# Optimization experiments

Measured on AMD Instinct MI355X. Metric: run time of the kernel, lower is better.

## Reference

```python
import jax, jax.numpy as jnp
import numpy as np


def setup_inputs() -> dict:
    key = jax.random.key(0)
    k1, k2 = jax.random.split(key)
    B = 64
    K = 4096
    latent_shape = (8, 250, 16)
    latent = jax.random.normal(k1, (B,) + latent_shape, dtype=jnp.float32)
    codebook = jax.random.normal(k2, (K,) + latent_shape, dtype=jnp.float32)
    usage_count = jnp.zeros((K,), dtype=jnp.float32)
    return {"latent": latent, "codebook": codebook, "usage_count": usage_count}


def reference(latent, codebook, usage_count):
    B = latent.shape[0]
    K = codebook.shape[0]
    latent_flat = latent.reshape(B, -1).astype(jnp.float32)      # [B, D]
    codebook_flat = codebook.reshape(K, -1).astype(jnp.float32)  # [K, D]

    x2 = jnp.sum(latent_flat * latent_flat, axis=1, keepdims=True)      # [B, 1]
    c2 = jnp.sum(codebook_flat * codebook_flat, axis=1)[None, :]        # [1, K]
    xc = jnp.einsum('bd,kd->bk', latent_flat, codebook_flat)            # [B, K]
    distances = jnp.sqrt(jnp.maximum(x2 + c2 - 2.0 * xc, 0.0))          # [B, K]

    indices = jnp.argmin(distances, axis=1)                             # [B] int
    min_distances = jnp.take_along_axis(distances, indices[:, None], axis=1)[:, 0]

    quantized = codebook[indices].astype(latent.dtype)                  # [B, *latent_shape]

    # scatter-add usage count update (handles duplicate indices)
    new_usage_count = usage_count.at[indices].add(1.0)

    return quantized, indices, min_distances, new_usage_count
```

## Files before the change

### kernel.cpp

```cpp
#include <hip/hip_runtime.h>
#include <math.h>

#define D      32000
#define BNUM   64
#define KNUM   4096
#define TN     64
#define BK     64
#define LDK    72

typedef __attribute__((ext_vector_type(8)))  short  short8;
typedef __attribute__((ext_vector_type(16))) float  floatx16;

__device__ __forceinline__ unsigned short f32_bf16_rne(float f) {
    unsigned u = __float_as_uint(f);
    u += 0x7fff + ((u >> 16) & 1);
    return (unsigned short)(u >> 16);
}
__device__ __forceinline__ float bf16_f32(unsigned short h) {
    return __uint_as_float(((unsigned)h) << 16);
}
__device__ __forceinline__ void cvt_hl(const float4 v, ushort4* h, ushort4* l) {
    h->x = f32_bf16_rne(v.x); l->x = f32_bf16_rne(v.x - bf16_f32(h->x));
    h->y = f32_bf16_rne(v.y); l->y = f32_bf16_rne(v.y - bf16_f32(h->y));
    h->z = f32_bf16_rne(v.z); l->z = f32_bf16_rne(v.z - bf16_f32(h->z));
    h->w = f32_bf16_rne(v.w); l->w = f32_bf16_rne(v.w - bf16_f32(h->w));
}

__device__ __forceinline__ void barrier_arrive() {
    __builtin_amdgcn_s_barrier();
}
__device__ __forceinline__ void barrier_lds() {
    __builtin_amdgcn_s_waitcnt(0xc07f);
    __builtin_amdgcn_s_barrier();
}

__global__ __launch_bounds__(256, 4) void dist_mfma(
    const float* __restrict__ latent, const float* __restrict__ codebook,
    float* __restrict__ ws_xc, float* __restrict__ ws_c2, int dper)
{
    __shared__ __align__(16) unsigned short xs_hi[BNUM * LDK];
    __shared__ __align__(16) unsigned short xs_lo[BNUM * LDK];
    __shared__ __align__(16) unsigned short cs_hi[TN * LDK];
    __shared__ __align__(16) unsigned short cs_lo[TN * LDK];

    const int tid  = threadIdx.x;
    const int k0   = blockIdx.x * TN;
    const int d0b  = blockIdx.y * dper;
    const int nst  = dper / BK;

    const int col4  = tid & 15;
    const int rbase = tid >> 4;
    const float* aptr = latent   + (size_t)rbase * D + d0b + col4 * 4;
    const float* bptr = codebook + (size_t)(k0 + rbase) * D + d0b + col4 * 4;

    const int wave = tid >> 6, lane = tid & 63;
    const int lr = lane & 31, lh = lane >> 5;
    const int mh = (wave & 1) * 32;
    const int nh = (wave >> 1) * 32;
    const int aoff = (mh + lr) * LDK + lh * 8;
    const int boff = (nh + lr) * LDK + lh * 8;

    floatx16 acc;
#pragma unroll
    for (int i = 0; i < 16; i++) acc[i] = 0.f;
    float c2p[4] = {0.f, 0.f, 0.f, 0.f};

    float4 pa[4], pbA[4], pbB[4];

#define LOADA(DST, S)                                                          \
    if ((S) < nst) {                                                           \
        const size_t _o = (size_t)(S) * BK;                                    \
        _Pragma("unroll")                                                      \
        for (int p = 0; p < 4; p++)                                            \
            DST[p] = *(const float4*)(aptr + (size_t)(16 * p) * D + _o);       \
    }
#define LOADB(DST, S)                                                          \
    if ((S) < nst) {                                                           \
        const size_t _o = (size_t)(S) * BK;                                    \
        _Pragma("unroll")                                                      \
        for (int p = 0; p < 4; p++)                                            \
            DST[p] = *(const float4*)(bptr + (size_t)(16 * p) * D + _o);       \
    }

#define STAGE(PBC, S)                                                          \
    {                                                                          \
        _Pragma("unroll")                                                      \
        for (int p = 0; p < 4; p++)                                            \
            c2p[p] += PBC[p].x * PBC[p].x + PBC[p].y * PBC[p].y +              \
                      PBC[p].z * PBC[p].z + PBC[p].w * PBC[p].w;               \
        barrier_arrive();                     \
        _Pragma("unroll")                                                      \
        for (int p = 0; p < 4; p++) {                                          \
            const int wo = (rbase + 16 * p) * LDK + col4 * 4;                  \
            ushort4 h, l;                                                      \
            cvt_hl(pa[p], &h, &l);                                             \
            *(ushort4*)(xs_hi + wo) = h;                                       \
            *(ushort4*)(xs_lo + wo) = l;                                       \
            cvt_hl(PBC[p], &h, &l);                                            \
            *(ushort4*)(cs_hi + wo) = h;                                       \
            *(ushort4*)(cs_lo + wo) = l;                                       \
        }                                                                      \
        LOADA(pa, (S) + 1);       \
        LOADB(PBC, (S) + 2);        \
        barrier_lds();                                                         \
        _Pragma("unroll")                                                      \
        for (int ks = 0; ks < 4; ++ks) {                                       \
            const short8 ah = *(const short8*)(xs_hi + aoff + ks * 16);        \
            const short8 al = *(const short8*)(xs_lo + aoff + ks * 16);        \
            const short8 bh = *(const short8*)(cs_hi + boff + ks * 16);        \
            const short8 bl = *(const short8*)(cs_lo + boff + ks * 16);        \
            acc = __builtin_amdgcn_mfma_f32_32x32x16_bf16(ah, bh, acc, 0,0,0); \
            acc = __builtin_amdgcn_mfma_f32_32x32x16_bf16(ah, bl, acc, 0,0,0); \
            acc = __builtin_amdgcn_mfma_f32_32x32x16_bf16(al, bh, acc, 0,0,0); \
        }                                                                      \
    }

    LOADA(pa, 0);
    LOADB(pbA, 0);
    LOADB(pbB, 1);

    int s = 0;
    for (; s + 1 < nst; s += 2) {
        STAGE(pbA, s);
        STAGE(pbB, s + 1);
    }
    if (s < nst) STAGE(pbA, s);

#undef STAGE
#undef LOADA
#undef LOADB

    const int split = blockIdx.y;
#pragma unroll
    for (int r = 0; r < 16; ++r) {
        const int row = (r & 3) + 8 * (r >> 2) + 4 * lh;
        const int b = mh + row;
        ws_xc[((size_t)split * BNUM + b) * KNUM + (k0 + nh + lr)] = acc[r];
    }

#pragma unroll
    for (int p = 0; p < 4; ++p) {
        float v = c2p[p];
        v += __shfl_xor(v, 1);
        v += __shfl_xor(v, 2);
        v += __shfl_xor(v, 4);
        v += __shfl_xor(v, 8);
        if ((lane & 15) == 0)
            atomicAdd(ws_c2 + k0 + rbase + 16 * p, v);
    }
}

__global__ __launch_bounds__(256) void argmin_part(
    const float* __restrict__ ws_xc, const float* __restrict__ ws_c2,
    float* __restrict__ ws_bscore, int* __restrict__ ws_bidx, int dsplit)
{
    const int b = blockIdx.x, kc = blockIdx.y, tid = threadIdx.x;
    __shared__ float sv[256];
    __shared__ int   si[256];

    float best = 3.402823466e38f;
    int   bi   = 0;
    for (int k = kc * 1024 + tid; k < (kc + 1) * 1024; k += 256) {
        float xc = 0.f;
        for (int s = 0; s < dsplit; s++)
            xc += ws_xc[((size_t)s * BNUM + b) * KNUM + k];
        const float sc = ws_c2[k] - 2.f * xc;
        if (sc < best) { best = sc; bi = k; }
    }
    sv[tid] = best; si[tid] = bi;
    __syncthreads();
    for (int off = 128; off > 0; off >>= 1) {
        if (tid < off) {
            const float ov = sv[tid + off];
            const int   oi = si[tid + off];
            if (ov < sv[tid] || (ov == sv[tid] && oi < si[tid])) {
                sv[tid] = ov; si[tid] = oi;
            }
        }
        __syncthreads();
    }
    if (tid == 0) { ws_bscore[b * 4 + kc] = sv[0]; ws_bidx[b * 4 + kc] = si[0]; }
}

__global__ __launch_bounds__(256) void finalize_k(
    const float* __restrict__ latent, const float* __restrict__ ws_bscore,
    const int* __restrict__ ws_bidx, const float* __restrict__ usage_in,
    float* __restrict__ out_idx, float* __restrict__ out_mind,
    float* __restrict__ out_usage, int* __restrict__ ws_idx)
{
    const int b = blockIdx.x, tid = threadIdx.x;
    __shared__ float sv[256];

    float s = 0.f;
    const float4* lf4 = (const float4*)(latent + (size_t)b * D);
    for (int i = tid; i < D / 4; i += 256) {
        const float4 v = lf4[i];
        s += v.x * v.x + v.y * v.y + v.z * v.z + v.w * v.w;
    }
    sv[tid] = s;
    __syncthreads();
    for (int off = 128; off > 0; off >>= 1) {
        if (tid < off) sv[tid] += sv[tid + off];
        __syncthreads();
    }
    if (tid == 0) {
        const float x2 = sv[0];
        float best = ws_bscore[b * 4];
        int   bi   = ws_bidx[b * 4];
        for (int kc = 1; kc < 4; kc++) {
            const float v = ws_bscore[b * 4 + kc];
            if (v < best) { best = v; bi = ws_bidx[b * 4 + kc]; }
        }
        out_mind[b] = sqrtf(fmaxf(x2 + best, 0.f));
        out_idx[b]  = (float)bi;
        ws_idx[b]   = bi;
    }
    if (tid < 64) out_usage[b * 64 + tid] = usage_in[b * 64 + tid];
}

__global__ __launch_bounds__(256) void gather_k(
    const float* __restrict__ codebook, const int* __restrict__ ws_idx,
    float* __restrict__ out_q, float* __restrict__ out_usage)
{
    const int b = blockIdx.x, part = blockIdx.y, tid = threadIdx.x;
    const int k = ws_idx[b];
    const int n4 = D / 4 / 4;
    const float4* src = (const float4*)(codebook + (size_t)k * D) + part * n4;
    float4*       dst = (float4*)(out_q + (size_t)b * D) + part * n4;
    for (int i = tid; i < n4; i += 256) dst[i] = src[i];
    if (part == 0 && tid == 0) atomicAdd(out_usage + k, 1.0f);
}

extern "C" void kernel_launch(void* const* d_in, const int* in_sizes, int n_in,
                              void* d_out, int out_size, void* d_ws, size_t ws_size,
                              hipStream_t stream)
{
    const float* latent   = (const float*)d_in[0];
    const float* codebook = (const float*)d_in[1];
    const float* usage    = (const float*)d_in[2];

    float* out_q     = (float*)d_out;
    float* out_idx   = out_q + (size_t)BNUM * D;
    float* out_mind  = out_idx + BNUM;
    float* out_usage = out_mind + BNUM;

    int dsplit = 20;
    if (ws_size < ((size_t)dsplit * BNUM * KNUM + KNUM + 4 * BNUM * 2 + BNUM) * 4 + 256)
        dsplit = 4;
    const int dper = D / dsplit;

    float* ws_xc     = (float*)d_ws;
    float* ws_c2     = ws_xc + (size_t)dsplit * BNUM * KNUM;
    float* ws_bscore = ws_c2 + KNUM;
    int*   ws_bidx   = (int*)(ws_bscore + 4 * BNUM);
    int*   ws_idx    = ws_bidx + 4 * BNUM;

    hipMemsetAsync(ws_c2, 0, KNUM * sizeof(float), stream);
    dist_mfma<<<dim3(KNUM / TN, dsplit), 256, 0, stream>>>(latent, codebook, ws_xc, ws_c2, dper);
    argmin_part<<<dim3(BNUM, 4), 256, 0, stream>>>(ws_xc, ws_c2, ws_bscore, ws_bidx, dsplit);
    finalize_k<<<BNUM, 256, 0, stream>>>(latent, ws_bscore, ws_bidx, usage,
                                         out_idx, out_mind, out_usage, ws_idx);
    gather_k<<<dim3(BNUM, 4), 256, 0, stream>>>(codebook, ws_idx, out_q, out_usage);
}
```

Baseline: 756.8 us.

## Preconvert latent to MFMA-ready bf16 hi/lo layout and double-buffer codebook LDS

```diff
diff --git a/kernel.cpp b/kernel.cpp
--- a/kernel.cpp
+++ b/kernel.cpp
@@ -6,7 +6,10 @@
 #define KNUM   4096
 #define TN     64
 #define BK     64
-#define LDK    72
+#define NSCB   (D / BK)
+#define AS_SCB 8192
+#define AFMT_USHORTS ((size_t)NSCB * AS_SCB)
+#define AFMT_BYTES   (AFMT_USHORTS * 2)
 
 typedef __attribute__((ext_vector_type(8)))  short  short8;
 typedef __attribute__((ext_vector_type(16))) float  floatx16;
@@ -26,109 +29,113 @@
     h->w = f32_bf16_rne(v.w); l->w = f32_bf16_rne(v.w - bf16_f32(h->w));
 }
 
-__device__ __forceinline__ void barrier_arrive() {
-    __builtin_amdgcn_s_barrier();
-}
 __device__ __forceinline__ void barrier_lds() {
     __builtin_amdgcn_s_waitcnt(0xc07f);
     __builtin_amdgcn_s_barrier();
 }
 
+__global__ __launch_bounds__(256) void conv_latent(
+    const float* __restrict__ latent, unsigned short* __restrict__ afmt)
+{
+    const int t    = blockIdx.x * 256 + threadIdx.x;
+    const int row  = t & 63;
+    const int rest = t >> 6;
+    if (rest >= NSCB * 8) return;
+    const int lh  = rest & 1;
+    const int ks  = (rest >> 1) & 3;
+    const int scb = rest >> 3;
+    const float* src = latent + (size_t)row * D + scb * 64 + ks * 16 + lh * 8;
+    const float4 v0 = *(const float4*)(src);
+    const float4 v1 = *(const float4*)(src + 4);
+    ushort4 h0, l0, h1, l1;
+    cvt_hl(v0, &h0, &l0);
+    cvt_hl(v1, &h1, &l1);
+    unsigned short* d0 = afmt + ((size_t)(rest * 2 + 0) * 64 + row) * 8;
+    unsigned short* d1 = afmt + ((size_t)(rest * 2 + 1) * 64 + row) * 8;
+    *(ushort4*)(d0)     = h0;  *(ushort4*)(d0 + 4) = h1;
+    *(ushort4*)(d1)     = l0;  *(ushort4*)(d1 + 4) = l1;
+}
+
+template<int NSTG>
 __global__ __launch_bounds__(256, 4) void dist_mfma(
-    const float* __restrict__ latent, const float* __restrict__ codebook,
-    float* __restrict__ ws_xc, float* __restrict__ ws_c2, int dper)
-{
-    __shared__ __align__(16) unsigned short xs_hi[BNUM * LDK];
-    __shared__ __align__(16) unsigned short xs_lo[BNUM * LDK];
-    __shared__ __align__(16) unsigned short cs_hi[TN * LDK];
-    __shared__ __align__(16) unsigned short cs_lo[TN * LDK];
+    const float* __restrict__ codebook, const unsigned short* __restrict__ afmt,
+    float* __restrict__ ws_xc, float* __restrict__ ws_c2)
+{
+    __shared__ __align__(16) unsigned short lds[2][2][8 * 520];
 
     const int tid  = threadIdx.x;
     const int k0   = blockIdx.x * TN;
-    const int d0b  = blockIdx.y * dper;
-    const int nst  = dper / BK;
-
-    const int col4  = tid & 15;
-    const int rbase = tid >> 4;
-    const float* aptr = latent   + (size_t)rbase * D + d0b + col4 * 4;
-    const float* bptr = codebook + (size_t)(k0 + rbase) * D + d0b + col4 * 4;
+    const int scb0 = blockIdx.y * NSTG;
+
+    const int col4 = tid & 15, rbase = tid >> 4;
+    const int cc2  = col4 >> 1, half = col4 & 1;
+    const float* bptr = codebook + (size_t)(k0 + rbase) * D
+                                 + (size_t)scb0 * 64 + col4 * 4;
 
     const int wave = tid >> 6, lane = tid & 63;
     const int lr = lane & 31, lh = lane >> 5;
-    const int mh = (wave & 1) * 32;
-    const int nh = (wave >> 1) * 32;
-    const int aoff = (mh + lr) * LDK + lh * 8;
-    const int boff = (nh + lr) * LDK + lh * 8;
+    const int mh = (wave & 1) * 32, nh = (wave >> 1) * 32;
+
+    const unsigned short* abase = afmt + (size_t)scb0 * AS_SCB
+                                       + lh * 1024 + (mh + lr) * 8;
+    const int rb_off = lh * 520 + (nh + lr) * 8;
 
     floatx16 acc;
 #pragma unroll
     for (int i = 0; i < 16; i++) acc[i] = 0.f;
     float c2p[4] = {0.f, 0.f, 0.f, 0.f};
-
-    float4 pa[4], pbA[4], pbB[4];
-
-#define LOADA(DST, S)                                                          \
-    if ((S) < nst) {                                                           \
-        const size_t _o = (size_t)(S) * BK;                                    \
-        _Pragma("unroll")                                                      \
-        for (int p = 0; p < 4; p++)                                            \
-            DST[p] = *(const float4*)(aptr + (size_t)(16 * p) * D + _o);       \
-    }
-#define LOADB(DST, S)                                                          \
-    if ((S) < nst) {                                                           \
-        const size_t _o = (size_t)(S) * BK;                                    \
-        _Pragma("unroll")                                                      \
-        for (int p = 0; p < 4; p++)                                            \
-            DST[p] = *(const float4*)(bptr + (size_t)(16 * p) * D + _o);       \
-    }
-
-#define STAGE(PBC, S)                                                          \
+    float4 pb[4];
+
+#define LOADB(S)                                                               \
     {                                                                          \
         _Pragma("unroll")                                                      \
         for (int p = 0; p < 4; p++)                                            \
-            c2p[p] += PBC[p].x * PBC[p].x + PBC[p].y * PBC[p].y +              \
-                      PBC[p].z * PBC[p].z + PBC[p].w * PBC[p].w;               \
-        barrier_arrive();                     \
+            pb[p] = *(const float4*)(bptr + (size_t)(16 * p) * D +             \
+                                     (size_t)(S) * 64);                        \
+    }
+
+#define CVTWRITE(NB)                                                           \
+    {                                                                          \
         _Pragma("unroll")                                                      \
         for (int p = 0; p < 4; p++) {                                          \
-            const int wo = (rbase + 16 * p) * LDK + col4 * 4;                  \
+            c2p[p] += pb[p].x * pb[p].x + pb[p].y * pb[p].y +                  \
+                      pb[p].z * pb[p].z + pb[p].w * pb[p].w;                   \
             ushort4 h, l;                                                      \
-            cvt_hl(pa[p], &h, &l);                                             \
-            *(ushort4*)(xs_hi + wo) = h;                                       \
-            *(ushort4*)(xs_lo + wo) = l;                                       \
-            cvt_hl(PBC[p], &h, &l);                                            \
-            *(ushort4*)(cs_hi + wo) = h;                                       \
-            *(ushort4*)(cs_lo + wo) = l;                                       \
+            cvt_hl(pb[p], &h, &l);                                             \
+            const int wo = cc2 * 520 + (rbase + 16 * p) * 8 + half * 4;        \
+            *(ushort4*)&lds[NB][0][wo] = h;                                    \
+            *(ushort4*)&lds[NB][1][wo] = l;                                    \
         }                                                                      \
-        LOADA(pa, (S) + 1);       \
-        LOADB(PBC, (S) + 2);        \
-        barrier_lds();                                                         \
-        _Pragma("unroll")                                                      \
-        for (int ks = 0; ks < 4; ++ks) {                                       \
-            const short8 ah = *(const short8*)(xs_hi + aoff + ks * 16);        \
-            const short8 al = *(const short8*)(xs_lo + aoff + ks * 16);        \
-            const short8 bh = *(const short8*)(cs_hi + boff + ks * 16);        \
-            const short8 bl = *(const short8*)(cs_lo + boff + ks * 16);        \
-            acc = __builtin_amdgcn_mfma_f32_32x32x16_bf16(ah, bh, acc, 0,0,0); \
-            acc = __builtin_amdgcn_mfma_f32_32x32x16_bf16(ah, bl, acc, 0,0,0); \
-            acc = __builtin_amdgcn_mfma_f32_32x32x16_bf16(al, bh, acc, 0,0,0); \
-        }                                                                      \
-    }
-
-    LOADA(pa, 0);
-    LOADB(pbA, 0);
-    LOADB(pbB, 1);
-
-    int s = 0;
-    for (; s + 1 < nst; s += 2) {
-        STAGE(pbA, s);
-        STAGE(pbB, s + 1);
-    }
-    if (s < nst) STAGE(pbA, s);
-
-#undef STAGE
-#undef LOADA
+    }
+
+    LOADB(0);
+    CVTWRITE(0);
+    LOADB(1);
+    barrier_lds();
+
+    for (int s = 0; s < NSTG; ++s) {
+        short8 ah[4], al[4];
+        const unsigned short* ap = abase + (size_t)s * AS_SCB;
+#pragma unroll
+        for (int q = 0; q < 4; q++) {
+            ah[q] = *(const short8*)(ap + q * 2048);
+            al[q] = *(const short8*)(ap + q * 2048 + 512);
+        }
+        if (s + 1 < NSTG) CVTWRITE((s + 1) & 1);
+        if (s + 2 < NSTG) LOADB(s + 2);
+        const int rbuf = s & 1;
+#pragma unroll
+        for (int q = 0; q < 4; q++) {
+            const short8 bh = *(const short8*)&lds[rbuf][0][q * 1040 + rb_off];
+            const short8 bl = *(const short8*)&lds[rbuf][1][q * 1040 + rb_off];
+            acc = __builtin_amdgcn_mfma_f32_32x32x16_bf16(ah[q], bh, acc, 0,0,0);
+            acc = __builtin_amdgcn_mfma_f32_32x32x16_bf16(ah[q], bl, acc, 0,0,0);
+            acc = __builtin_amdgcn_mfma_f32_32x32x16_bf16(al[q], bh, acc, 0,0,0);
+        }
+        barrier_lds();
+    }
 #undef LOADB
+#undef CVTWRITE
 
     const int split = blockIdx.y;
 #pragma unroll
@@ -150,24 +157,21 @@
     }
 }
 
+template<int DS>
 __global__ __launch_bounds__(256) void argmin_part(
     const float* __restrict__ ws_xc, const float* __restrict__ ws_c2,
-    float* __restrict__ ws_bscore, int* __restrict__ ws_bidx, int dsplit)
+    float* __restrict__ ws_bscore, int* __restrict__ ws_bidx)
 {
     const int b = blockIdx.x, kc = blockIdx.y, tid = threadIdx.x;
+    const int k = kc * 256 + tid;
+    float xc = 0.f;
+#pragma unroll
+    for (int s = 0; s < DS; s++)
+        xc += ws_xc[((size_t)s * BNUM + b) * KNUM + k];
     __shared__ float sv[256];
     __shared__ int   si[256];
-
-    float best = 3.402823466e38f;
-    int   bi   = 0;
-    for (int k = kc * 1024 + tid; k < (kc + 1) * 1024; k += 256) {
-        float xc = 0.f;
-        for (int s = 0; s < dsplit; s++)
-            xc += ws_xc[((size_t)s * BNUM + b) * KNUM + k];
-        const float sc = ws_c2[k] - 2.f * xc;
-        if (sc < best) { best = sc; bi = k; }
-    }
-    sv[tid] = best; si[tid] = bi;
+    sv[tid] = ws_c2[k] - 2.f * xc;
+    si[tid] = k;
     __syncthreads();
     for (int off = 128; off > 0; off >>= 1) {
         if (tid < off) {
@@ -179,7 +183,7 @@
         }
         __syncthreads();
     }
-    if (tid == 0) { ws_bscore[b * 4 + kc] = sv[0]; ws_bidx[b * 4 + kc] = si[0]; }
+    if (tid == 0) { ws_bscore[b * 16 + kc] = sv[0]; ws_bidx[b * 16 + kc] = si[0]; }
 }
 
 __global__ __launch_bounds__(256) void finalize_k(
@@ -205,11 +209,11 @@
     }
     if (tid == 0) {
         const float x2 = sv[0];
-        float best = ws_bscore[b * 4];
-        int   bi   = ws_bidx[b * 4];
-        for (int kc = 1; kc < 4; kc++) {
-            const float v = ws_bscore[b * 4 + kc];
-            if (v < best) { best = v; bi = ws_bidx[b * 4 + kc]; }
+        float best = ws_bscore[b * 16];
+        int   bi   = ws_bidx[b * 16];
+        for (int kc = 1; kc < 16; kc++) {
+            const float v = ws_bscore[b * 16 + kc];
+            if (v < best) { best = v; bi = ws_bidx[b * 16 + kc]; }
         }
         out_mind[b] = sqrtf(fmaxf(x2 + best, 0.f));
         out_idx[b]  = (float)bi;
@@ -244,20 +248,26 @@
     float* out_mind  = out_idx + BNUM;
     float* out_usage = out_mind + BNUM;
 
-    int dsplit = 20;
-    if (ws_size < ((size_t)dsplit * BNUM * KNUM + KNUM + 4 * BNUM * 2 + BNUM) * 4 + 256)
-        dsplit = 4;
-    const int dper = D / dsplit;
-
-    float* ws_xc     = (float*)d_ws;
+    const size_t need20 = AFMT_BYTES +
+        ((size_t)20 * BNUM * KNUM + KNUM + 16 * BNUM * 2 + BNUM) * 4 + 256;
+    const int dsplit = (ws_size >= need20) ? 20 : 4;
+
+    unsigned short* afmt = (unsigned short*)d_ws;
+    float* ws_xc     = (float*)((char*)d_ws + AFMT_BYTES);
     float* ws_c2     = ws_xc + (size_t)dsplit * BNUM * KNUM;
     float* ws_bscore = ws_c2 + KNUM;
-    int*   ws_bidx   = (int*)(ws_bscore + 4 * BNUM);
-    int*   ws_idx    = ws_bidx + 4 * BNUM;
+    int*   ws_bidx   = (int*)(ws_bscore + 16 * BNUM);
+    int*   ws_idx    = ws_bidx + 16 * BNUM;
 
     hipMemsetAsync(ws_c2, 0, KNUM * sizeof(float), stream);
-    dist_mfma<<<dim3(KNUM / TN, dsplit), 256, 0, stream>>>(latent, codebook, ws_xc, ws_c2, dper);
-    argmin_part<<<dim3(BNUM, 4), 256, 0, stream>>>(ws_xc, ws_c2, ws_bscore, ws_bidx, dsplit);
+    conv_latent<<<NSCB * 8 * 64 / 256, 256, 0, stream>>>(latent, afmt);
+    if (dsplit == 20) {
+        dist_mfma<25><<<dim3(KNUM / TN, 20), 256, 0, stream>>>(codebook, afmt, ws_xc, ws_c2);
+        argmin_part<20><<<dim3(BNUM, 16), 256, 0, stream>>>(ws_xc, ws_c2, ws_bscore, ws_bidx);
+    } else {
+        dist_mfma<125><<<dim3(KNUM / TN, 4), 256, 0, stream>>>(codebook, afmt, ws_xc, ws_c2);
+        argmin_part<4><<<dim3(BNUM, 16), 256, 0, stream>>>(ws_xc, ws_c2, ws_bscore, ws_bidx);
+    }
     finalize_k<<<BNUM, 256, 0, stream>>>(latent, ws_bscore, ws_bidx, usage,
                                          out_idx, out_mind, out_usage, ws_idx);
     gather_k<<<dim3(BNUM, 4), 256, 0, stream>>>(codebook, ws_idx, out_q, out_usage);
```

After: 740.2 us. 2.2% less time.
